# Kernel tuning notes

Hardware: AMD Instinct MI355X
Metric: run time of the kernel (lower is better)

## Reference

```python
import jax, jax.numpy as jnp
import numpy as np

# --- fan-beam geometry (matches init_kwargs geometry dict) ---
VOL = 256            # volume is VOL x VOL pixels
SPACING = 1.0        # volume pixel spacing (world units)
N_PROJ = 256         # number of projection angles
N_DET = 384          # detector pixel count
DET_SPACING = 1.2    # detector pixel spacing
ANG_RANGE = 2.0 * np.pi
SID = 400.0          # source-isocenter distance
SDD = 800.0          # source-detector distance
N_SAMPLES = 256      # samples along each ray (covers volume diagonal)


def _ray_sample_points():
    """World-space sample points along each (angle, detector-pixel) ray.
    Returns pts [P, D, S, 2] and the step length dt."""
    theta = jnp.arange(N_PROJ, dtype=jnp.float32) * (ANG_RANGE / N_PROJ)
    cen = jnp.stack([jnp.cos(theta), jnp.sin(theta)], axis=-1)     # central ray dir [P,2]
    u = jnp.stack([-jnp.sin(theta), jnp.cos(theta)], axis=-1)      # detector axis  [P,2]
    src = -SID * cen                                               # source position [P,2]
    det_off = (jnp.arange(N_DET, dtype=jnp.float32) - (N_DET - 1) / 2.0) * DET_SPACING
    # flat detector pixel positions [P,D,2]
    det = src[:, None, :] + SDD * cen[:, None, :] + det_off[None, :, None] * u[:, None, :]
    ray = det - src[:, None, :]
    ray = ray / jnp.linalg.norm(ray, axis=-1, keepdims=True)       # unit ray dirs [P,D,2]
    diag = SPACING * VOL * np.sqrt(2.0)                            # volume diagonal
    dt = jnp.float32(diag / N_SAMPLES)
    # sample the segment of each ray that can intersect the volume
    t = SID - diag / 2.0 + (jnp.arange(N_SAMPLES, dtype=jnp.float32) + 0.5) * dt  # [S]
    pts = src[:, None, None, :] + t[None, None, :, None] * ray[:, :, None, :]     # [P,D,S,2]
    return pts, dt


def _bilinear(img, pts):
    """Bilinear interpolation of img [H,W] at world points pts [...,2]; zero outside."""
    x = pts[..., 0] / SPACING + (VOL - 1) / 2.0   # fractional column index
    y = pts[..., 1] / SPACING + (VOL - 1) / 2.0   # fractional row index
    x0 = jnp.floor(x)
    y0 = jnp.floor(y)
    wx = x - x0
    y_w = y - y0
    x0i = x0.astype(jnp.int32)
    y0i = y0.astype(jnp.int32)

    def tap(yi, xi):
        inb = (xi >= 0) & (xi < VOL) & (yi >= 0) & (yi < VOL)
        v = img[jnp.clip(yi, 0, VOL - 1), jnp.clip(xi, 0, VOL - 1)]
        return jnp.where(inb, v, 0.0)

    return ((1 - wx) * (1 - y_w) * tap(y0i, x0i)
            + wx * (1 - y_w) * tap(y0i, x0i + 1)
            + (1 - wx) * y_w * tap(y0i + 1, x0i)
            + wx * y_w * tap(y0i + 1, x0i + 1))


def setup_inputs() -> dict:
    key = jax.random.key(0)
    x = jax.random.normal(key, (2, VOL, VOL, 1), dtype=jnp.float32)
    return {"x": x}


def reference(x):
    """Fan-beam forward projection: x [B,H,W,1] -> sinogram [B,P,D,1]."""
    pts, dt = _ray_sample_points()                 # [P,D,S,2], scalar

    def project_one(im):                           # im [H,W] -> sino [P,D]
        return _bilinear(im, pts).sum(axis=-1) * dt

    sino = jax.vmap(project_one)(x[..., 0])       # [B,P,D]
    return sino[..., None]                         # [B,P,D,1]
```

## Files before the change

### kernel.cpp

```cpp
#include <hip/hip_runtime.h>
#include <hip/hip_fp16.h>

#define VOL    256
#define NPROJ  256
#define NDET   384
#define NS     256
#define PROW   129
#define PDWN   (258 * PROW)
#define PDW    33284
#define PV4    (PDW / 4)
#define NBATCH 2
#define TPB    768

typedef _Float16 hvec2 __attribute__((ext_vector_type(2)));

#if defined(__has_builtin)
#if __has_builtin(__builtin_amdgcn_fdot2)
#define HAS_FDOT2 1
#endif
#endif

__global__ void pad_build_kernel(const float* __restrict__ src, uint* __restrict__ dst) {
    int idx = blockIdx.x * blockDim.x + threadIdx.x;
    if (idx >= NBATCH * PDW) return;
    int b = idx / PDW;
    int d = idx - b * PDW;
    uint val = 0u;
    if (d < PDWN) {
        int uy = d / PROW;
        int q  = d - uy * PROW;
        int r  = uy - 1;
        int c0 = 2 * q - 1;
        const float* im = src + (b << 16);
        float v0 = 0.0f, v1 = 0.0f;
        if ((unsigned)r < 256u) {
            const float* rp = im + (r << 8);
            if ((unsigned)c0 < 256u)       v0 = rp[c0];
            if ((unsigned)(c0 + 1) < 256u) v1 = rp[c0 + 1];
        }
        __half2 h = __floats2half2_rn(v0, v1);
        val = *reinterpret_cast<uint*>(&h);
    }
    dst[idx] = val;
}

__global__ __launch_bounds__(TPB) void fanproj_kernel(const uint4* __restrict__ G,
                                                      float* __restrict__ out) {
    __shared__ uint4 s4[PV4];
    const uint* sImg = reinterpret_cast<const uint*>(s4);

    int tid = threadIdx.x;
    int ray = blockIdx.x * TPB + tid;
    int b   = blockIdx.x >> 7;

    {
        const uint4* gb = G + (size_t)b * PV4;
        for (int i = tid; i < PV4; i += TPB) s4[i] = gb[i];
    }

    int d  = ray % NDET;
    int pb = ray / NDET;
    int p  = pb & (NPROJ - 1);

    const float dt = 1.4142135623730951f;
    const float t0 = 219.68777079743137f;

    float theta = (float)p * (6.283185307179586f / (float)NPROJ);
    float st, ct;
    __sincosf(theta, &st, &ct);

    float srcx = -400.0f * ct;
    float srcy = -400.0f * st;
    float off  = ((float)d - 191.5f) * 1.2f;
    float rx   = fmaf(800.0f, ct, -off * st);
    float ry   = fmaf(800.0f, st,  off * ct);
    float n2   = rx * rx + ry * ry;
    float rn   = rsqrtf(n2);
    rn = rn * (1.5f - 0.5f * n2 * rn * rn);
    rx *= rn;
    ry *= rn;

    float bxu = fmaf(t0, rx, srcx) + 128.5f;
    float byu = fmaf(t0, ry, srcy) + 128.5f;
    float sx  = dt * rx;
    float sy  = dt * ry;

    const float EPS = 2e-3f;
    float sxs = (fabsf(sx) < 1e-9f) ? copysignf(1e-9f, sx) : sx;
    float sys = (fabsf(sy) < 1e-9f) ? copysignf(1e-9f, sy) : sy;
    float isx = 1.0f / sxs;
    float isy = 1.0f / sys;
    float ax0 = (0.0f   - bxu) * isx, ax1 = (257.0f - bxu) * isx;
    float ay0 = (0.0f   - byu) * isy, ay1 = (257.0f - byu) * isy;
    float lo  = fmaxf(fminf(ax0, ax1), fminf(ay0, ay1)) + EPS;
    float hi  = fminf(fmaxf(ax0, ax1), fmaxf(ay0, ay1)) - EPS;
    lo = fminf(fmaxf(lo, -1.0f), 300.0f);
    hi = fminf(fmaxf(hi, -1.0f), 300.0f);
    int slo = max(0,      (int)ceilf(lo));
    int shi = min(NS - 1, (int)floorf(hi));

    __syncthreads();

    float acc = 0.0f;
    float sf  = (float)slo;
    for (int s = slo; s <= shi; ++s) {
        float X = fmaf(sf, sx, bxu);
        float Y = fmaf(sf, sy, byu);
        sf += 1.0f;
        float Xf = floorf(X);
        float Yf = floorf(Y);
        float wx = X - Xf;
        float wy = Y - Yf;
        int ux = (int)Xf;
        int uy = (int)Yf;
        int base = uy * PROW + (ux >> 1);
        uint d0 = sImg[base];
        uint d1 = sImg[base + 1];
        uint d2 = sImg[base + PROW];
        uint d3 = sImg[base + PROW + 1];
        unsigned sh = (unsigned)(ux & 1) << 4;
        uint tw = __builtin_amdgcn_alignbit(d1, d0, sh);
        uint bw = __builtin_amdgcn_alignbit(d3, d2, sh);
#ifdef HAS_FDOT2
        hvec2 hx = __builtin_bit_cast(hvec2, __builtin_amdgcn_cvt_pkrtz(1.0f - wx, wx));
        hvec2 tv = __builtin_bit_cast(hvec2, tw);
        hvec2 bv = __builtin_bit_cast(hvec2, bw);
        float top = __builtin_amdgcn_fdot2(tv, hx, 0.0f, false);
        float bot = __builtin_amdgcn_fdot2(bv, hx, 0.0f, false);
        acc = fmaf(wy, bot - top, acc + top);
#else
        __half2 ht = *reinterpret_cast<__half2*>(&tw);
        __half2 hb = *reinterpret_cast<__half2*>(&bw);
        float2 rt = __half22float2(ht);
        float2 rb = __half22float2(hb);
        float top = fmaf(wx, rt.y - rt.x, rt.x);
        float bot = fmaf(wx, rb.y - rb.x, rb.x);
        acc = fmaf(wy, bot - top, acc + top);
#endif
    }
    out[ray] = acc * dt;
}

extern "C" void kernel_launch(void* const* d_in, const int* in_sizes, int n_in,
                              void* d_out, int out_size, void* d_ws, size_t ws_size,
                              hipStream_t stream) {
    const float* x = (const float*)d_in[0];
    float* out     = (float*)d_out;
    uint* hpad     = (uint*)d_ws;

    int ndw = NBATCH * PDW;
    pad_build_kernel<<<(ndw + 255) / 256, 256, 0, stream>>>(x, hpad);

    fanproj_kernel<<<256, TPB, 0, stream>>>((const uint4*)hpad, out);
}
```

Measured before the change: 89.67 us.

## Split image into two row halves per block and combine rays with atomics

The padded half-precision image is split into two overlapping row bands, each small enough to halve the shared memory per block. The projector launches twice as many blocks, and each block integrates only the part of its ray that falls inside its band. Partial sums are combined with atomic adds into an output zeroed by a memset. This aims to double block count and occupancy across CUs, at the cost of an extra memset, redundant per-ray setup, atomics and less balanced work per half.

```diff
diff --git a/kernel.cpp b/kernel.cpp
--- a/kernel.cpp
+++ b/kernel.cpp
@@ -6,9 +6,10 @@
 #define NDET   384
 #define NS     256
 #define PROW   129
-#define PDWN   (258 * PROW)
-#define PDW    33284
-#define PV4    (PDW / 4)
+#define PHR    132
+#define PHD    (PHR * PROW)
+#define PH4    (PHD / 4)
+#define ROWB   126
 #define NBATCH 2
 #define TPB    768
 
@@ -22,40 +23,39 @@
 
 __global__ void pad_build_kernel(const float* __restrict__ src, uint* __restrict__ dst) {
     int idx = blockIdx.x * blockDim.x + threadIdx.x;
-    if (idx >= NBATCH * PDW) return;
-    int b = idx / PDW;
-    int d = idx - b * PDW;
-    uint val = 0u;
-    if (d < PDWN) {
-        int uy = d / PROW;
-        int q  = d - uy * PROW;
-        int r  = uy - 1;
-        int c0 = 2 * q - 1;
-        const float* im = src + (b << 16);
-        float v0 = 0.0f, v1 = 0.0f;
-        if ((unsigned)r < 256u) {
-            const float* rp = im + (r << 8);
-            if ((unsigned)c0 < 256u)       v0 = rp[c0];
-            if ((unsigned)(c0 + 1) < 256u) v1 = rp[c0 + 1];
-        }
-        __half2 h = __floats2half2_rn(v0, v1);
-        val = *reinterpret_cast<uint*>(&h);
+    if (idx >= NBATCH * 2 * PHD) return;
+    int bh   = idx / PHD;
+    int dd   = idx - bh * PHD;
+    int rowl = dd / PROW;
+    int q    = dd - rowl * PROW;
+    int uy   = rowl + (bh & 1) * ROWB;
+    int r    = uy - 1;
+    int c0   = 2 * q - 1;
+    const float* im = src + ((bh >> 1) << 16);
+    float v0 = 0.0f, v1 = 0.0f;
+    if ((unsigned)r < 256u) {
+        const float* rp = im + (r << 8);
+        if ((unsigned)c0 < 256u)       v0 = rp[c0];
+        if ((unsigned)(c0 + 1) < 256u) v1 = rp[c0 + 1];
     }
-    dst[idx] = val;
+    __half2 h2 = __floats2half2_rn(v0, v1);
+    dst[idx] = *reinterpret_cast<uint*>(&h2);
 }
 
 __global__ __launch_bounds__(TPB) void fanproj_kernel(const uint4* __restrict__ G,
                                                       float* __restrict__ out) {
-    __shared__ uint4 s4[PV4];
+    __shared__ uint4 s4[PH4];
     const uint* sImg = reinterpret_cast<const uint*>(s4);
 
     int tid = threadIdx.x;
-    int ray = blockIdx.x * TPB + tid;
-    int b   = blockIdx.x >> 7;
+    int h   = blockIdx.x & 1;
+    int grp = blockIdx.x >> 1;
+    int ray = grp * TPB + tid;
+    int b   = grp >> 7;
 
     {
-        const uint4* gb = G + (size_t)b * PV4;
-        for (int i = tid; i < PV4; i += TPB) s4[i] = gb[i];
+        const uint4* gb = G + (size_t)((b << 1) + h) * PH4;
+        for (int i = tid; i < PH4; i += TPB) s4[i] = gb[i];
     }
 
     int d  = ray % NDET;
@@ -90,8 +90,8 @@
     float sys = (fabsf(sy) < 1e-9f) ? copysignf(1e-9f, sy) : sy;
     float isx = 1.0f / sxs;
     float isy = 1.0f / sys;
-    float ax0 = (0.0f   - bxu) * isx, ax1 = (257.0f - bxu) * isx;
-    float ay0 = (0.0f   - byu) * isy, ay1 = (257.0f - byu) * isy;
+    float ax0 = (0.0f - bxu) * isx, ax1 = (257.0f - bxu) * isx;
+    float ay0 = (0.0f - byu) * isy, ay1 = (257.0f - byu) * isy;
     float lo  = fmaxf(fminf(ax0, ax1), fminf(ay0, ay1)) + EPS;
     float hi  = fminf(fmaxf(ax0, ax1), fmaxf(ay0, ay1)) - EPS;
     lo = fminf(fmaxf(lo, -1.0f), 300.0f);
@@ -99,11 +99,26 @@
     int slo = max(0,      (int)ceilf(lo));
     int shi = min(NS - 1, (int)floorf(hi));
 
+    float tS = (129.0f - byu) * isy;
+    tS = fminf(fmaxf(tS, -2.0f), 300.0f);
+    int  kUp = (int)ceilf(tS);
+    int  kDn = (int)floorf(tS) + 1;
+    bool pos = (sys > 0.0f);
+    int myLo, myHi;
+    if (h == 0) {
+        myLo = pos ? slo : max(slo, kDn);
+        myHi = pos ? min(shi, kUp - 1) : shi;
+    } else {
+        myLo = pos ? max(slo, kUp) : slo;
+        myHi = pos ? shi : min(shi, kDn - 1);
+    }
+    if (h) byu -= (float)ROWB;
+
     __syncthreads();
 
     float acc = 0.0f;
-    float sf  = (float)slo;
-    for (int s = slo; s <= shi; ++s) {
+    float sf  = (float)myLo;
+    for (int s = myLo; s <= myHi; ++s) {
         float X = fmaf(sf, sx, bxu);
         float Y = fmaf(sf, sy, byu);
         sf += 1.0f;
@@ -138,7 +153,7 @@
         acc = fmaf(wy, bot - top, acc + top);
 #endif
     }
-    out[ray] = acc * dt;
+    if (myLo <= myHi) atomicAdd(&out[ray], acc * dt);
 }
 
 extern "C" void kernel_launch(void* const* d_in, const int* in_sizes, int n_in,
@@ -148,8 +163,10 @@
     float* out     = (float*)d_out;
     uint* hpad     = (uint*)d_ws;
 
-    int ndw = NBATCH * PDW;
+    hipMemsetAsync(out, 0, (size_t)out_size * sizeof(float), stream);
+
+    int ndw = NBATCH * 2 * PHD;
     pad_build_kernel<<<(ndw + 255) / 256, 256, 0, stream>>>(x, hpad);
 
-    fanproj_kernel<<<256, TPB, 0, stream>>>((const uint4*)hpad, out);
+    fanproj_kernel<<<512, TPB, 0, stream>>>((const uint4*)hpad, out);
 }
```

Result: no change. 89.74 us (+0.1%).
